# Kernel optimization log

Measured on AMD Instinct MI355X. Metric: run time of the kernel, lower is better.

## Reference

```python
import jax, jax.numpy as jnp
import numpy as np

N = 50000   # nodes
E = 800000  # edges
H = 128     # hidden_dim
K = 4       # Chebyshev order
EPS_BN = 1e-5
EPS_L2 = 1e-12


def setup_inputs() -> dict:
    key = jax.random.key(0)
    ks = jax.random.split(key, 8)
    x = jax.random.normal(ks[0], (N, 3), dtype=jnp.float32)
    edge_index = jax.random.randint(ks[1], (2, E), 0, N, dtype=jnp.int32)

    def lin(k, fi, fo):
        s = 1.0 / np.sqrt(fi)
        return jax.random.uniform(k, (fi, fo), jnp.float32, -s, s)

    def cheb_params(k, fi, fo):
        kk = jax.random.split(k, K)
        W = jnp.stack([lin(kk[i], fi, fo) for i in range(K)])  # [K, fi, fo]
        b = jnp.zeros((fo,), jnp.float32)
        return W, b

    W1, b1 = cheb_params(ks[2], 3, H)
    W2, b2 = cheb_params(ks[3], H, H)
    W3, b3 = cheb_params(ks[4], H, H)
    W4, b4 = cheb_params(ks[5], H, H)
    Wr = lin(ks[6], H, 3)
    br = jnp.zeros((3,), jnp.float32)
    ones = jnp.ones((H,), jnp.float32)
    zeros = jnp.zeros((H,), jnp.float32)
    return {
        'x': x, 'edge_index': edge_index,
        'W1': W1, 'b1': b1, 'W2': W2, 'b2': b2,
        'W3': W3, 'b3': b3, 'W4': W4, 'b4': b4,
        'g1': ones, 'be1': zeros, 'g2': ones, 'be2': zeros,
        'g3': ones, 'be3': zeros, 'Wr': Wr, 'br': br,
    }


def _prop(h, src, dst, norm):
    # one sparse Laplacian application: out[dst] += norm * h[src]
    return jax.ops.segment_sum(norm[:, None] * h[src], dst, num_segments=N)


def _cheb(h, src, dst, norm, W, b):
    # PyG ChebConv with sym normalization, lambda_max=2 -> L_hat edge weights
    # are -D^-1/2 A D^-1/2 with zero diagonal (encoded in norm).
    out = h @ W[0]
    Tx0, Tx1 = h, _prop(h, src, dst, norm)
    out = out + Tx1 @ W[1]
    for k in range(2, W.shape[0]):
        Tx2 = 2.0 * _prop(Tx1, src, dst, norm) - Tx0
        out = out + Tx2 @ W[k]
        Tx0, Tx1 = Tx1, Tx2
    return out + b


def _bn(h, g, b):
    # BatchNorm1d in training mode: batch stats over node dim, biased var
    m = h.mean(axis=0)
    v = h.var(axis=0)
    return g * (h - m) * jax.lax.rsqrt(v + EPS_BN) + b


def reference(x, edge_index, W1, b1, W2, b2, W3, b3, W4, b4,
              g1, be1, g2, be2, g3, be3, Wr, br):
    src, dst = edge_index[0], edge_index[1]
    deg = jax.ops.segment_sum(jnp.ones((E,), jnp.float32), src, num_segments=N)
    dinv = jnp.where(deg > 0, jax.lax.rsqrt(jnp.maximum(deg, 1.0)), 0.0)
    norm = -dinv[src] * dinv[dst]

    h = _bn(jax.nn.leaky_relu(_cheb(x, src, dst, norm, W1, b1)), g1, be1)
    h = _bn(jax.nn.leaky_relu(_cheb(h, src, dst, norm, W2, b2)), g2, be2)
    h = _bn(jax.nn.relu(_cheb(h, src, dst, norm, W3, b3)), g3, be3)
    h = _cheb(h, src, dst, norm, W4, b4)
    # F.normalize(p=2, dim=1)
    h = h / jnp.maximum(jnp.linalg.norm(h, axis=1, keepdims=True), EPS_L2)
    return h @ Wr + br
```

## Files before the change

### kernel.cpp

```cpp
#include <hip/hip_runtime.h>
#include <hip/hip_fp16.h>

#define HD 128

typedef __attribute__((ext_vector_type(8))) short bf16x8;
typedef __attribute__((ext_vector_type(4))) float f32x4;
typedef unsigned int u32;

struct h4s { __half2 a, b; };

__device__ __forceinline__ float lrelu(float x, float s) { return x > 0.f ? x : s * x; }

__device__ __forceinline__ u32 bf16rtne(float x) {
  u32 u = __float_as_uint(x);
  return (u + 0x7fffu + ((u >> 16) & 1u)) >> 16;
}

__global__ void k_edge_count(const int* __restrict__ src, const int* __restrict__ dst,
                             int* __restrict__ degc, int* __restrict__ cnt, int E) {
  int e = blockIdx.x * blockDim.x + threadIdx.x;
  if (e < E) {
    atomicAdd(&degc[src[e]], 1);
    atomicAdd(&cnt[dst[e]], 1);
  }
}

__global__ __launch_bounds__(1024) void k_scan1(const int* __restrict__ cnt,
                                                int* __restrict__ rowptr,
                                                int* __restrict__ bsums, int n) {
  __shared__ int buf[1024];
  int i = blockIdx.x * 1024 + threadIdx.x;
  int v = (i < n) ? cnt[i] : 0;
  buf[threadIdx.x] = v;
  __syncthreads();
  for (int o = 1; o < 1024; o <<= 1) {
    int t = (threadIdx.x >= (unsigned)o) ? buf[threadIdx.x - o] : 0;
    __syncthreads();
    buf[threadIdx.x] += t;
    __syncthreads();
  }
  if (i < n) rowptr[i] = buf[threadIdx.x] - v;
  if (threadIdx.x == 1023) bsums[blockIdx.x] = buf[1023];
}

__global__ __launch_bounds__(1024) void k_scan3(int* __restrict__ rowptr, int* __restrict__ wo,
                                                const int* __restrict__ bsums,
                                                const int* __restrict__ degc,
                                                float* __restrict__ dinv, int n, int Etot,
                                                int nb) {
  __shared__ int blockoff;
  if (nb <= 64) {
    if (threadIdx.x < 64) {
      int lane = threadIdx.x;
      int v = (lane < nb) ? bsums[lane] : 0;
      int inc = v;
#pragma unroll
      for (int o = 1; o < 64; o <<= 1) {
        int t = __shfl_up(inc, o, 64);
        if (lane >= o) inc += t;
      }
      if (lane == (int)blockIdx.x) blockoff = inc - v;
    }
  } else if (threadIdx.x == 0) {
    int sum = 0;
    for (int t = 0; t < (int)blockIdx.x; ++t) sum += bsums[t];
    blockoff = sum;
  }
  __syncthreads();
  int i = blockIdx.x * 1024 + threadIdx.x;
  if (i < n) {
    int r = rowptr[i] + blockoff;
    rowptr[i] = r;
    wo[i] = r;
    int dg = degc[i];
    dinv[i] = dg > 0 ? rsqrtf((float)dg) : 0.f;
  }
  if (i == 0) rowptr[n] = Etot;
}

__global__ void k_fill(const int* __restrict__ src, const int* __restrict__ dst,
                       int* __restrict__ wo, const float* __restrict__ dinv,
                       uint2* __restrict__ cw, int E) {
  int e = blockIdx.x * blockDim.x + threadIdx.x;
  if (e < E) {
    int s = src[e], d = dst[e];
    int p = atomicAdd(&wo[d], 1);
    cw[p] = make_uint2((u32)s, __float_as_uint(-dinv[s] * dinv[d]));
  }
}

__global__ void k_prop3(const int* __restrict__ rowptr, const uint2* __restrict__ cw,
                        const float* __restrict__ Hs, const float* __restrict__ Sub,
                        float* __restrict__ Out, float scale, int n) {
  int r = blockIdx.x * blockDim.x + threadIdx.x;
  if (r >= n) return;
  int b = rowptr[r], e = rowptr[r + 1];
  float a0 = 0.f, a1 = 0.f, a2 = 0.f;
  for (int j = b; j < e; ++j) {
    uint2 m = cw[j];
    int s = (int)m.x;
    float w = __uint_as_float(m.y);
    a0 = fmaf(w, Hs[s * 3 + 0], a0);
    a1 = fmaf(w, Hs[s * 3 + 1], a1);
    a2 = fmaf(w, Hs[s * 3 + 2], a2);
  }
  float r0 = scale * a0, r1 = scale * a1, r2 = scale * a2;
  if (Sub) { r0 -= Sub[r * 3 + 0]; r1 -= Sub[r * 3 + 1]; r2 -= Sub[r * 3 + 2]; }
  Out[r * 3 + 0] = r0; Out[r * 3 + 1] = r1; Out[r * 3 + 2] = r2;
}

template <int PHI>
__global__ __launch_bounds__(256) void k_prop128(
    const int* __restrict__ rowptr, const uint2* __restrict__ cw,
    const __half* __restrict__ Ph, const float* __restrict__ Sub,
    float* __restrict__ Out, __half* __restrict__ Outh, float scale, int n,
    const float* __restrict__ gsc, const float* __restrict__ gsh,
    const float* __restrict__ ssc, const float* __restrict__ ssh, float slope) {
  int r = blockIdx.x * 4 + (int)(threadIdx.x >> 6);
  int lane = threadIdx.x & 63;
  if (r >= n) return;
  int b = rowptr[r], e = rowptr[r + 1];
  int fl = (lane & 31) << 2;
  int half = lane >> 5;
  float ax = 0.f, ay = 0.f, az = 0.f, aw = 0.f, ws = 0.f;
  int j = b;
  for (; j + 7 < e; j += 8) {
    h4s h[4];
    float w[4];
#pragma unroll
    for (int q = 0; q < 4; ++q) {
      int idx = j + 2 * q + half;
      uint2 m = cw[idx];
      w[q] = __uint_as_float(m.y);
      h[q] = *(const h4s*)&Ph[(size_t)m.x * HD + fl];
    }
#pragma unroll
    for (int q = 0; q < 4; ++q) {
      float2 f0 = __half22float2(h[q].a);
      float2 f1 = __half22float2(h[q].b);
      if (PHI) {
        f0.x = lrelu(f0.x, slope); f0.y = lrelu(f0.y, slope);
        f1.x = lrelu(f1.x, slope); f1.y = lrelu(f1.y, slope);
        ws += w[q];
      }
      ax = fmaf(w[q], f0.x, ax);
      ay = fmaf(w[q], f0.y, ay);
      az = fmaf(w[q], f1.x, az);
      aw = fmaf(w[q], f1.y, aw);
    }
  }
  for (; j + 1 < e; j += 2) {
    int idx = j + half;
    uint2 m = cw[idx];
    float w = __uint_as_float(m.y);
    h4s h = *(const h4s*)&Ph[(size_t)m.x * HD + fl];
    float2 f0 = __half22float2(h.a);
    float2 f1 = __half22float2(h.b);
    if (PHI) {
      f0.x = lrelu(f0.x, slope); f0.y = lrelu(f0.y, slope);
      f1.x = lrelu(f1.x, slope); f1.y = lrelu(f1.y, slope);
      ws += w;
    }
    ax = fmaf(w, f0.x, ax);
    ay = fmaf(w, f0.y, ay);
    az = fmaf(w, f1.x, az);
    aw = fmaf(w, f1.y, aw);
  }
  if (j < e && half == 0) {
    uint2 m = cw[j];
    float w = __uint_as_float(m.y);
    h4s h = *(const h4s*)&Ph[(size_t)m.x * HD + fl];
    float2 f0 = __half22float2(h.a);
    float2 f1 = __half22float2(h.b);
    if (PHI) {
      f0.x = lrelu(f0.x, slope); f0.y = lrelu(f0.y, slope);
      f1.x = lrelu(f1.x, slope); f1.y = lrelu(f1.y, slope);
      ws += w;
    }
    ax = fmaf(w, f0.x, ax);
    ay = fmaf(w, f0.y, ay);
    az = fmaf(w, f1.x, az);
    aw = fmaf(w, f1.y, aw);
  }
  ax += __shfl_xor(ax, 32, 64);
  ay += __shfl_xor(ay, 32, 64);
  az += __shfl_xor(az, 32, 64);
  aw += __shfl_xor(aw, 32, 64);
  if (PHI) {
    ws += __shfl_xor(ws, 32, 64);
    float4 g4 = *(const float4*)&gsc[fl];
    float4 s4 = *(const float4*)&gsh[fl];
    ax = fmaf(ax, g4.x, ws * s4.x);
    ay = fmaf(ay, g4.y, ws * s4.y);
    az = fmaf(az, g4.z, ws * s4.z);
    aw = fmaf(aw, g4.w, ws * s4.w);
  }
  float4 o = make_float4(scale * ax, scale * ay, scale * az, scale * aw);
  if (Sub) {
    float4 sb = *(const float4*)&Sub[(size_t)r * HD + fl];
    if (ssc != nullptr) {
      float4 c4 = *(const float4*)&ssc[fl];
      float4 d4 = *(const float4*)&ssh[fl];
      sb.x = fmaf(lrelu(sb.x, slope), c4.x, d4.x);
      sb.y = fmaf(lrelu(sb.y, slope), c4.y, d4.y);
      sb.z = fmaf(lrelu(sb.z, slope), c4.z, d4.z);
      sb.w = fmaf(lrelu(sb.w, slope), c4.w, d4.w);
    }
    o.x -= sb.x; o.y -= sb.y; o.z -= sb.z; o.w -= sb.w;
  }
  if (half == 0) {
    *(float4*)&Out[(size_t)r * HD + fl] = o;
    if (Outh) {
      h4s ho;
      ho.a = __float22half2_rn(make_float2(o.x, o.y));
      ho.b = __float22half2_rn(make_float2(o.z, o.w));
      *(h4s*)&Outh[(size_t)r * HD + fl] = ho;
    }
  }
}

__global__ __launch_bounds__(128) void k_l1gemm(
    const float* __restrict__ X, const float* __restrict__ T1, const float* __restrict__ T2,
    const float* __restrict__ T3, const float* __restrict__ W1, const float* __restrict__ b1,
    float* __restrict__ Out, __half* __restrict__ Outh,
    float* __restrict__ bnsum, float* __restrict__ bnsq,
    float slope, int n, int rpb) {
  int j = threadIdx.x;
  float w[12];
#pragma unroll
  for (int t = 0; t < 4; ++t)
#pragma unroll
    for (int c = 0; c < 3; ++c) w[t * 3 + c] = W1[(t * 3 + c) * HD + j];
  float bj = b1[j];
  int r0 = blockIdx.x * rpb, r1 = min(r0 + rpb, n);
  float s = 0.f, q = 0.f;
  for (int r = r0; r < r1; ++r) {
    float acc = bj;
#pragma unroll
    for (int c = 0; c < 3; ++c) {
      acc = fmaf(X [r * 3 + c], w[0 + c], acc);
      acc = fmaf(T1[r * 3 + c], w[3 + c], acc);
      acc = fmaf(T2[r * 3 + c], w[6 + c], acc);
      acc = fmaf(T3[r * 3 + c], w[9 + c], acc);
    }
    Out[(size_t)r * HD + j] = acc;
    Outh[(size_t)r * HD + j] = __float2half(acc);
    float a = lrelu(acc, slope);
    s += a;
    q = fmaf(a, a, q);
  }
  atomicAdd(&bnsum[j], s);
  atomicAdd(&bnsq[j], q);
}

__global__ void k_wsplit3(const float* __restrict__ W2, const float* __restrict__ W3,
                          const float* __restrict__ W4, uint4* __restrict__ Whi,
                          uint4* __restrict__ Wlo) {
  int flat = blockIdx.x * 256 + threadIdx.x;
  int wsel = flat >> 13;
  int f = flat & 8191;
  const float* W = (wsel == 0) ? W2 : (wsel == 1) ? W3 : W4;
  int n = f & 127, K8 = f >> 7;
  int chunk = K8 >> 2, g = K8 & 3;
  bf16x8 hv, lv;
#pragma unroll
  for (int i = 0; i < 8; ++i) {
    int k = chunk * 32 + ((i >> 2) << 4) + g * 4 + (i & 3);
    float v = W[(size_t)k * HD + n];
    u32 hb = bf16rtne(v);
    float hf = __uint_as_float(hb << 16);
    u32 lb = bf16rtne(v - hf);
    hv[i] = (short)hb;
    lv[i] = (short)lb;
  }
  int slot = chunk * 512 + (n >> 4) * 64 + g * 16 + (n & 15);
  Whi[wsel * 8192 + slot] = *(uint4*)&hv;
  Wlo[wsel * 8192 + slot] = *(uint4*)&lv;
}

__global__ __launch_bounds__(256) void k_gemm4m(
    const float* __restrict__ T0, const float* __restrict__ T1,
    const float* __restrict__ T2, const float* __restrict__ T3,
    const uint4* __restrict__ Whi, const uint4* __restrict__ Wlo,
    const float* __restrict__ bias, float* __restrict__ OUT, __half* __restrict__ OUTh,
    float* bnsum, float* bnsq, float stat_slope,
    const float* __restrict__ gsc, const float* __restrict__ gsh, float phi_slope,
    int nrows) {
  __shared__ short sAh[2048], sAl[2048];
  __shared__ short sWh[4096], sWl[4096];
  __shared__ float redS[128], redQ[128];

  int tid = threadIdx.x;
  int lane = tid & 63, w = tid >> 6, wr = w >> 1, wc = w & 1;
  int g = (tid >> 4) & 3;
  int ri = tid & 15;
  int row0 = blockIdx.x * 64;
  int arow = row0 + w * 16 + ri;
  bool aval = arow < nrows;

  f32x4 zero = {0.f, 0.f, 0.f, 0.f};
  f32x4 acc[2][4];
#pragma unroll
  for (int mi = 0; mi < 2; ++mi)
#pragma unroll
    for (int nj = 0; nj < 4; ++nj) acc[mi][nj] = zero;

  if (tid < 128) { redS[tid] = 0.f; redQ[tid] = 0.f; }

  for (int chunk = 0; chunk < 16; ++chunk) {
    const float* Ts = (chunk < 4) ? T0 : (chunk < 8) ? T1 : (chunk < 12) ? T2 : T3;
    int kc = chunk & 3;
    float4 va = make_float4(0.f, 0.f, 0.f, 0.f), vb = va;
    if (aval) {
      const float* ap = Ts + (size_t)arow * HD + kc * 32 + g * 4;
      va = *(const float4*)ap;
      vb = *(const float4*)(ap + 16);
    }
    size_t wbase = (size_t)chunk * 512;
    uint4 wh0 = Whi[wbase + tid], wh1 = Whi[wbase + 256 + tid];
    uint4 wl0 = Wlo[wbase + tid], wl1 = Wlo[wbase + 256 + tid];

    __syncthreads();

    float vals[8] = {va.x, va.y, va.z, va.w, vb.x, vb.y, vb.z, vb.w};
    if (gsc != nullptr && chunk < 4) {
#pragma unroll
      for (int i = 0; i < 8; ++i) {
        int f = kc * 32 + g * 4 + (i & 3) + ((i >> 2) << 4);
        vals[i] = fmaf(lrelu(vals[i], phi_slope), gsc[f], gsh[f]);
      }
    }
    bf16x8 hv, lv;
#pragma unroll
    for (int i = 0; i < 8; ++i) {
      u32 hb = bf16rtne(vals[i]);
      float hf = __uint_as_float(hb << 16);
      u32 lb = bf16rtne(vals[i] - hf);
      hv[i] = (short)hb;
      lv[i] = (short)lb;
    }
    *(bf16x8*)&sAh[tid * 8] = hv;
    *(bf16x8*)&sAl[tid * 8] = lv;
    *(uint4*)&sWh[tid * 8] = wh0;
    *(uint4*)&sWh[(256 + tid) * 8] = wh1;
    *(uint4*)&sWl[tid * 8] = wl0;
    *(uint4*)&sWl[(256 + tid) * 8] = wl1;
    __syncthreads();

    bf16x8 ah[2], al[2], bh[4], bl[4];
#pragma unroll
    for (int mi = 0; mi < 2; ++mi) {
      ah[mi] = *(const bf16x8*)&sAh[((wr * 2 + mi) * 64 + lane) * 8];
      al[mi] = *(const bf16x8*)&sAl[((wr * 2 + mi) * 64 + lane) * 8];
    }
#pragma unroll
    for (int nj = 0; nj < 4; ++nj) {
      bh[nj] = *(const bf16x8*)&sWh[((wc * 4 + nj) * 64 + lane) * 8];
      bl[nj] = *(const bf16x8*)&sWl[((wc * 4 + nj) * 64 + lane) * 8];
    }
#pragma unroll
    for (int mi = 0; mi < 2; ++mi)
#pragma unroll
      for (int nj = 0; nj < 4; ++nj) {
        acc[mi][nj] = __builtin_amdgcn_mfma_f32_16x16x32_bf16(ah[mi], bh[nj], acc[mi][nj], 0, 0, 0);
        acc[mi][nj] = __builtin_amdgcn_mfma_f32_16x16x32_bf16(ah[mi], bl[nj], acc[mi][nj], 0, 0, 0);
        acc[mi][nj] = __builtin_amdgcn_mfma_f32_16x16x32_bf16(al[mi], bh[nj], acc[mi][nj], 0, 0, 0);
      }
  }

  int l4 = (lane >> 4) * 4, ni = lane & 15;
  bool stats = (bnsum != nullptr);
#pragma unroll
  for (int nj = 0; nj < 4; ++nj) {
    int c = wc * 64 + nj * 16 + ni;
    float bcol = bias[c];
    float s = 0.f, q = 0.f;
#pragma unroll
    for (int mi = 0; mi < 2; ++mi)
#pragma unroll
      for (int j = 0; j < 4; ++j) {
        int row = row0 + (wr * 2 + mi) * 16 + l4 + j;
        if (row < nrows) {
          float v = acc[mi][nj][j] + bcol;
          OUT[(size_t)row * HD + c] = v;
          if (OUTh) OUTh[(size_t)row * HD + c] = __float2half(v);
          if (stats) {
            float a = lrelu(v, stat_slope);
            s += a;
            q = fmaf(a, a, q);
          }
        }
      }
    if (stats) {
      s += __shfl_xor(s, 16, 64);
      s += __shfl_xor(s, 32, 64);
      q += __shfl_xor(q, 16, 64);
      q += __shfl_xor(q, 32, 64);
      if (lane < 16) {
        atomicAdd(&redS[c], s);
        atomicAdd(&redQ[c], q);
      }
    }
  }
  if (stats) {
    __syncthreads();
    if (tid < 128) {
      atomicAdd(&bnsum[tid], redS[tid]);
      atomicAdd(&bnsq[tid], redQ[tid]);
    }
  }
}

__global__ void k_bnfin(const float* __restrict__ bsum, const float* __restrict__ bsq,
                        const float* __restrict__ g, const float* __restrict__ be,
                        float* __restrict__ scaleb, float* __restrict__ shiftb, int n) {
  int f = threadIdx.x;
  if (f < HD) {
    float m = bsum[f] / (float)n;
    float v = bsq[f] / (float)n - m * m;
    float rs = rsqrtf(v + 1e-5f);
    float sc = g[f] * rs;
    scaleb[f] = sc;
    shiftb[f] = be[f] - m * sc;
  }
}

__global__ __launch_bounds__(256) void k_final(const float* __restrict__ Hb,
                                               const float* __restrict__ Wr,
                                               const float* __restrict__ br,
                                               float* __restrict__ out, int n) {
  int r = blockIdx.x * 4 + (int)(threadIdx.x >> 6);
  int lane = threadIdx.x & 63;
  if (r >= n) return;
  float h0 = Hb[(size_t)r * HD + lane];
  float h1 = Hb[(size_t)r * HD + 64 + lane];
  float ss = h0 * h0 + h1 * h1;
#pragma unroll
  for (int o = 32; o; o >>= 1) ss += __shfl_xor(ss, o, 64);
  float inv = 1.f / fmaxf(sqrtf(ss), 1e-12f);
  h0 *= inv; h1 *= inv;
  float o0 = h0 * Wr[lane * 3 + 0] + h1 * Wr[(64 + lane) * 3 + 0];
  float o1 = h0 * Wr[lane * 3 + 1] + h1 * Wr[(64 + lane) * 3 + 1];
  float o2 = h0 * Wr[lane * 3 + 2] + h1 * Wr[(64 + lane) * 3 + 2];
#pragma unroll
  for (int o = 32; o; o >>= 1) {
    o0 += __shfl_xor(o0, o, 64);
    o1 += __shfl_xor(o1, o, 64);
    o2 += __shfl_xor(o2, o, 64);
  }
  if (lane == 0) {
    out[r * 3 + 0] = o0 + br[0];
    out[r * 3 + 1] = o1 + br[1];
    out[r * 3 + 2] = o2 + br[2];
  }
}

extern "C" void kernel_launch(void* const* d_in, const int* in_sizes, int n_in,
                              void* d_out, int out_size, void* d_ws, size_t ws_size,
                              hipStream_t stream) {
  const float* x  = (const float*)d_in[0];
  const int*   ei = (const int*)d_in[1];
  const float* W1 = (const float*)d_in[2];
  const float* b1 = (const float*)d_in[3];
  const float* W2 = (const float*)d_in[4];
  const float* b2 = (const float*)d_in[5];
  const float* W3 = (const float*)d_in[6];
  const float* b3 = (const float*)d_in[7];
  const float* W4 = (const float*)d_in[8];
  const float* b4 = (const float*)d_in[9];
  const float* g1 = (const float*)d_in[10];
  const float* be1= (const float*)d_in[11];
  const float* g2 = (const float*)d_in[12];
  const float* be2= (const float*)d_in[13];
  const float* g3 = (const float*)d_in[14];
  const float* be3= (const float*)d_in[15];
  const float* Wr = (const float*)d_in[16];
  const float* br = (const float*)d_in[17];

  const int N = in_sizes[0] / 3;
  const int E = in_sizes[1] / 2;
  const int* src = ei;
  const int* dst = ei + E;
  float* out = (float*)d_out;

  char* wp = (char*)d_ws;
  size_t used = 0;
  auto alloc = [&](size_t bytes) -> void* {
    void* p = (void*)(wp + used);
    used += (bytes + 255) & ~(size_t)255;
    return p;
  };
  int*   deg2   = (int*)alloc((size_t)2 * N * 4);
  int*   rowptr = (int*)alloc((size_t)(N + 1) * 4);
  int*   wo     = (int*)alloc((size_t)N * 4);
  float* dinv   = (float*)alloc((size_t)N * 4);
  int*   bsums  = (int*)alloc(256 * 4);
  uint2* cw     = (uint2*)alloc((size_t)E * 8);
  float* t1     = (float*)alloc((size_t)N * 3 * 4);
  float* t2     = (float*)alloc((size_t)N * 3 * 4);
  float* t3     = (float*)alloc((size_t)N * 3 * 4);
  float* buf0   = (float*)alloc((size_t)N * HD * 4);
  float* buf1   = (float*)alloc((size_t)N * HD * 4);
  float* buf2   = (float*)alloc((size_t)N * HD * 4);
  float* buf3   = (float*)alloc((size_t)N * HD * 4);
  __half* phA   = (__half*)alloc((size_t)N * HD * 2);
  __half* phB   = (__half*)alloc((size_t)N * HD * 2);
  float* stats  = (float*)alloc(6 * HD * 4);
  float* scsh   = (float*)alloc(6 * HD * 4);
  uint4* Whi3   = (uint4*)alloc(3 * 8192 * 16);
  uint4* Wlo3   = (uint4*)alloc(3 * 8192 * 16);
  if (used > ws_size) return;

  int* degc = deg2;
  int* cnt  = deg2 + N;
  float* bnsum1 = stats + 0 * HD; float* bnsq1 = stats + 1 * HD;
  float* bnsum2 = stats + 2 * HD; float* bnsq2 = stats + 3 * HD;
  float* bnsum3 = stats + 4 * HD; float* bnsq3 = stats + 5 * HD;
  float* sc1 = scsh + 0 * HD; float* sh1 = scsh + 1 * HD;
  float* sc2 = scsh + 2 * HD; float* sh2 = scsh + 3 * HD;
  float* sc3 = scsh + 4 * HD; float* sh3 = scsh + 5 * HD;

  const int eb = (E + 255) / 256;
  const int nb = (N + 255) / 256;
  const int pb = (N + 3) / 4;
  const int sb = (N + 1023) / 1024;
  const int gbm = (N + 63) / 64;

  hipMemsetAsync(stats, 0, 6 * HD * 4, stream);
  hipMemsetAsync(deg2, 0, (size_t)2 * N * 4, stream);
  k_edge_count<<<eb, 256, 0, stream>>>(src, dst, degc, cnt, E);
  k_scan1<<<sb, 1024, 0, stream>>>(cnt, rowptr, bsums, N);
  k_scan3<<<sb, 1024, 0, stream>>>(rowptr, wo, bsums, degc, dinv, N, E, sb);
  k_fill<<<eb, 256, 0, stream>>>(src, dst, wo, dinv, cw, E);
  k_wsplit3<<<96, 256, 0, stream>>>(W2, W3, W4, Whi3, Wlo3);

  k_prop3<<<nb, 256, 0, stream>>>(rowptr, cw, x, nullptr, t1, 1.f, N);
  k_prop3<<<nb, 256, 0, stream>>>(rowptr, cw, t1, x, t2, 2.f, N);
  k_prop3<<<nb, 256, 0, stream>>>(rowptr, cw, t2, t1, t3, 2.f, N);
  k_l1gemm<<<(N + 255) / 256, 128, 0, stream>>>(x, t1, t2, t3, W1, b1, buf0, phA,
                                                bnsum1, bnsq1, 0.01f, N, 256);
  k_bnfin<<<1, 128, 0, stream>>>(bnsum1, bnsq1, g1, be1, sc1, sh1, N);

  auto cheb_layer = [&](const uint4* Whi, const uint4* Wlo, const float* bk,
                        const float* psc, const float* psh, float phi_slope,
                        float* bs, float* bq, float stat_slope, bool last) {
    k_prop128<1><<<pb, 256, 0, stream>>>(rowptr, cw, phA, nullptr, buf1, phB, 1.f, N,
                                         psc, psh, nullptr, nullptr, phi_slope);
    k_prop128<0><<<pb, 256, 0, stream>>>(rowptr, cw, phB, buf0, buf2, phA, 2.f, N,
                                         nullptr, nullptr, psc, psh, phi_slope);
    k_prop128<0><<<pb, 256, 0, stream>>>(rowptr, cw, phA, buf1, buf3, nullptr, 2.f, N,
                                         nullptr, nullptr, nullptr, nullptr, 0.f);
    k_gemm4m<<<gbm, 256, 0, stream>>>(buf0, buf1, buf2, buf3, Whi, Wlo, bk, buf0,
                                      last ? nullptr : phA,
                                      bs, bq, stat_slope, psc, psh, phi_slope, N);
  };

  cheb_layer(Whi3, Wlo3, b2, sc1, sh1, 0.01f, bnsum2, bnsq2, 0.01f, false);
  k_bnfin<<<1, 128, 0, stream>>>(bnsum2, bnsq2, g2, be2, sc2, sh2, N);
  cheb_layer(Whi3 + 8192, Wlo3 + 8192, b3, sc2, sh2, 0.01f, bnsum3, bnsq3, 0.0f, false);
  k_bnfin<<<1, 128, 0, stream>>>(bnsum3, bnsq3, g3, be3, sc3, sh3, N);
  cheb_layer(Whi3 + 16384, Wlo3 + 16384, b4, sc3, sh3, 0.0f, nullptr, nullptr, 0.0f, true);

  k_final<<<pb, 256, 0, stream>>>(buf0, Wr, br, out, N);
}
```

Before: 721.2 us.

## Store all Chebyshev intermediates in fp16 and drop atomic CSR fill

Removes the fp32 copies of the Chebyshev intermediates. The propagation, GEMM and final kernels now read and write only fp16 buffers (four half buffers rotated per layer), roughly halving intermediate memory traffic. The CSR build also records each edge's slot from the counting atomic, so the fill pass computes positions without a second atomic. This trades some precision, since the subtracted terms and the GEMM inputs are now fp16-rounded, and adds an E-sized index buffer.

Result: faster. 684.8 us (-5.0%).

```diff
diff --git a/kernel.cpp b/kernel.cpp
--- a/kernel.cpp
+++ b/kernel.cpp
@@ -17,11 +17,12 @@
 }
 
 __global__ void k_edge_count(const int* __restrict__ src, const int* __restrict__ dst,
-                             int* __restrict__ degc, int* __restrict__ cnt, int E) {
+                             int* __restrict__ degc, int* __restrict__ cnt,
+                             int* __restrict__ ledge, int E) {
   int e = blockIdx.x * blockDim.x + threadIdx.x;
   if (e < E) {
     atomicAdd(&degc[src[e]], 1);
-    atomicAdd(&cnt[dst[e]], 1);
+    ledge[e] = atomicAdd(&cnt[dst[e]], 1);
   }
 }
 
@@ -43,7 +44,7 @@
   if (threadIdx.x == 1023) bsums[blockIdx.x] = buf[1023];
 }
 
-__global__ __launch_bounds__(1024) void k_scan3(int* __restrict__ rowptr, int* __restrict__ wo,
+__global__ __launch_bounds__(1024) void k_scan3(int* __restrict__ rowptr,
                                                 const int* __restrict__ bsums,
                                                 const int* __restrict__ degc,
                                                 float* __restrict__ dinv, int n, int Etot,
@@ -69,9 +70,7 @@
   __syncthreads();
   int i = blockIdx.x * 1024 + threadIdx.x;
   if (i < n) {
-    int r = rowptr[i] + blockoff;
-    rowptr[i] = r;
-    wo[i] = r;
+    rowptr[i] += blockoff;
     int dg = degc[i];
     dinv[i] = dg > 0 ? rsqrtf((float)dg) : 0.f;
   }
@@ -79,12 +78,12 @@
 }
 
 __global__ void k_fill(const int* __restrict__ src, const int* __restrict__ dst,
-                       int* __restrict__ wo, const float* __restrict__ dinv,
-                       uint2* __restrict__ cw, int E) {
+                       const int* __restrict__ ledge, const int* __restrict__ rowptr,
+                       const float* __restrict__ dinv, uint2* __restrict__ cw, int E) {
   int e = blockIdx.x * blockDim.x + threadIdx.x;
   if (e < E) {
     int s = src[e], d = dst[e];
-    int p = atomicAdd(&wo[d], 1);
+    int p = rowptr[d] + ledge[e];
     cw[p] = make_uint2((u32)s, __float_as_uint(-dinv[s] * dinv[d]));
   }
 }
@@ -112,8 +111,8 @@
 template <int PHI>
 __global__ __launch_bounds__(256) void k_prop128(
     const int* __restrict__ rowptr, const uint2* __restrict__ cw,
-    const __half* __restrict__ Ph, const float* __restrict__ Sub,
-    float* __restrict__ Out, __half* __restrict__ Outh, float scale, int n,
+    const __half* __restrict__ Ph, const __half* __restrict__ Sub,
+    __half* __restrict__ Outh, float scale, int n,
     const float* __restrict__ gsc, const float* __restrict__ gsh,
     const float* __restrict__ ssc, const float* __restrict__ ssh, float slope) {
   int r = blockIdx.x * 4 + (int)(threadIdx.x >> 6);
@@ -197,33 +196,31 @@
   }
   float4 o = make_float4(scale * ax, scale * ay, scale * az, scale * aw);
   if (Sub) {
-    float4 sb = *(const float4*)&Sub[(size_t)r * HD + fl];
+    h4s sh4 = *(const h4s*)&Sub[(size_t)r * HD + fl];
+    float2 s0 = __half22float2(sh4.a);
+    float2 s1 = __half22float2(sh4.b);
     if (ssc != nullptr) {
       float4 c4 = *(const float4*)&ssc[fl];
       float4 d4 = *(const float4*)&ssh[fl];
-      sb.x = fmaf(lrelu(sb.x, slope), c4.x, d4.x);
-      sb.y = fmaf(lrelu(sb.y, slope), c4.y, d4.y);
-      sb.z = fmaf(lrelu(sb.z, slope), c4.z, d4.z);
-      sb.w = fmaf(lrelu(sb.w, slope), c4.w, d4.w);
-    }
-    o.x -= sb.x; o.y -= sb.y; o.z -= sb.z; o.w -= sb.w;
+      s0.x = fmaf(lrelu(s0.x, slope), c4.x, d4.x);
+      s0.y = fmaf(lrelu(s0.y, slope), c4.y, d4.y);
+      s1.x = fmaf(lrelu(s1.x, slope), c4.z, d4.z);
+      s1.y = fmaf(lrelu(s1.y, slope), c4.w, d4.w);
+    }
+    o.x -= s0.x; o.y -= s0.y; o.z -= s1.x; o.w -= s1.y;
   }
   if (half == 0) {
-    *(float4*)&Out[(size_t)r * HD + fl] = o;
-    if (Outh) {
-      h4s ho;
-      ho.a = __float22half2_rn(make_float2(o.x, o.y));
-      ho.b = __float22half2_rn(make_float2(o.z, o.w));
-      *(h4s*)&Outh[(size_t)r * HD + fl] = ho;
-    }
+    h4s ho;
+    ho.a = __float22half2_rn(make_float2(o.x, o.y));
+    ho.b = __float22half2_rn(make_float2(o.z, o.w));
+    *(h4s*)&Outh[(size_t)r * HD + fl] = ho;
   }
 }
 
 __global__ __launch_bounds__(128) void k_l1gemm(
     const float* __restrict__ X, const float* __restrict__ T1, const float* __restrict__ T2,
     const float* __restrict__ T3, const float* __restrict__ W1, const float* __restrict__ b1,
-    float* __restrict__ Out, __half* __restrict__ Outh,
-    float* __restrict__ bnsum, float* __restrict__ bnsq,
+    __half* __restrict__ Outh, float* __restrict__ bnsum, float* __restrict__ bnsq,
     float slope, int n, int rpb) {
   int j = threadIdx.x;
   float w[12];
@@ -243,7 +240,6 @@
       acc = fmaf(T2[r * 3 + c], w[6 + c], acc);
       acc = fmaf(T3[r * 3 + c], w[9 + c], acc);
     }
-    Out[(size_t)r * HD + j] = acc;
     Outh[(size_t)r * HD + j] = __float2half(acc);
     float a = lrelu(acc, slope);
     s += a;
@@ -279,10 +275,10 @@
 }
 
 __global__ __launch_bounds__(256) void k_gemm4m(
-    const float* __restrict__ T0, const float* __restrict__ T1,
-    const float* __restrict__ T2, const float* __restrict__ T3,
+    const __half* __restrict__ T0, const __half* __restrict__ T1,
+    const __half* __restrict__ T2, const __half* __restrict__ T3,
     const uint4* __restrict__ Whi, const uint4* __restrict__ Wlo,
-    const float* __restrict__ bias, float* __restrict__ OUT, __half* __restrict__ OUTh,
+    const float* __restrict__ bias, __half* __restrict__ OUTh,
     float* bnsum, float* bnsq, float stat_slope,
     const float* __restrict__ gsc, const float* __restrict__ gsh, float phi_slope,
     int nrows) {
@@ -308,13 +304,17 @@
   if (tid < 128) { redS[tid] = 0.f; redQ[tid] = 0.f; }
 
   for (int chunk = 0; chunk < 16; ++chunk) {
-    const float* Ts = (chunk < 4) ? T0 : (chunk < 8) ? T1 : (chunk < 12) ? T2 : T3;
+    const __half* Ts = (chunk < 4) ? T0 : (chunk < 8) ? T1 : (chunk < 12) ? T2 : T3;
     int kc = chunk & 3;
-    float4 va = make_float4(0.f, 0.f, 0.f, 0.f), vb = va;
+    float vals[8] = {0.f, 0.f, 0.f, 0.f, 0.f, 0.f, 0.f, 0.f};
     if (aval) {
-      const float* ap = Ts + (size_t)arow * HD + kc * 32 + g * 4;
-      va = *(const float4*)ap;
-      vb = *(const float4*)(ap + 16);
+      const __half* ap = Ts + (size_t)arow * HD + kc * 32 + g * 4;
+      h4s va = *(const h4s*)ap;
+      h4s vb = *(const h4s*)(ap + 16);
+      float2 f0 = __half22float2(va.a), f1 = __half22float2(va.b);
+      float2 f2 = __half22float2(vb.a), f3 = __half22float2(vb.b);
+      vals[0] = f0.x; vals[1] = f0.y; vals[2] = f1.x; vals[3] = f1.y;
+      vals[4] = f2.x; vals[5] = f2.y; vals[6] = f3.x; vals[7] = f3.y;
     }
     size_t wbase = (size_t)chunk * 512;
     uint4 wh0 = Whi[wbase + tid], wh1 = Whi[wbase + 256 + tid];
@@ -322,7 +322,6 @@
 
     __syncthreads();
 
-    float vals[8] = {va.x, va.y, va.z, va.w, vb.x, vb.y, vb.z, vb.w};
     if (gsc != nullptr && chunk < 4) {
 #pragma unroll
       for (int i = 0; i < 8; ++i) {
@@ -382,8 +381,7 @@
         int row = row0 + (wr * 2 + mi) * 16 + l4 + j;
         if (row < nrows) {
           float v = acc[mi][nj][j] + bcol;
-          OUT[(size_t)row * HD + c] = v;
-          if (OUTh) OUTh[(size_t)row * HD + c] = __float2half(v);
+          OUTh[(size_t)row * HD + c] = __float2half(v);
           if (stats) {
             float a = lrelu(v, stat_slope);
             s += a;
@@ -425,15 +423,15 @@
   }
 }
 
-__global__ __launch_bounds__(256) void k_final(const float* __restrict__ Hb,
+__global__ __launch_bounds__(256) void k_final(const __half* __restrict__ Hb,
                                                const float* __restrict__ Wr,
                                                const float* __restrict__ br,
                                                float* __restrict__ out, int n) {
   int r = blockIdx.x * 4 + (int)(threadIdx.x >> 6);
   int lane = threadIdx.x & 63;
   if (r >= n) return;
-  float h0 = Hb[(size_t)r * HD + lane];
-  float h1 = Hb[(size_t)r * HD + 64 + lane];
+  float h0 = __half2float(Hb[(size_t)r * HD + lane]);
+  float h1 = __half2float(Hb[(size_t)r * HD + 64 + lane]);
   float ss = h0 * h0 + h1 * h1;
 #pragma unroll
   for (int o = 32; o; o >>= 1) ss += __shfl_xor(ss, o, 64);
@@ -492,19 +490,17 @@
   };
   int*   deg2   = (int*)alloc((size_t)2 * N * 4);
   int*   rowptr = (int*)alloc((size_t)(N + 1) * 4);
-  int*   wo     = (int*)alloc((size_t)N * 4);
   float* dinv   = (float*)alloc((size_t)N * 4);
   int*   bsums  = (int*)alloc(256 * 4);
+  int*   ledge  = (int*)alloc((size_t)E * 4);
   uint2* cw     = (uint2*)alloc((size_t)E * 8);
   float* t1     = (float*)alloc((size_t)N * 3 * 4);
   float* t2     = (float*)alloc((size_t)N * 3 * 4);
   float* t3     = (float*)alloc((size_t)N * 3 * 4);
-  float* buf0   = (float*)alloc((size_t)N * HD * 4);
-  float* buf1   = (float*)alloc((size_t)N * HD * 4);
-  float* buf2   = (float*)alloc((size_t)N * HD * 4);
-  float* buf3   = (float*)alloc((size_t)N * HD * 4);
   __half* phA   = (__half*)alloc((size_t)N * HD * 2);
   __half* phB   = (__half*)alloc((size_t)N * HD * 2);
+  __half* phC   = (__half*)alloc((size_t)N * HD * 2);
+  __half* phD   = (__half*)alloc((size_t)N * HD * 2);
   float* stats  = (float*)alloc(6 * HD * 4);
   float* scsh   = (float*)alloc(6 * HD * 4);
   uint4* Whi3   = (uint4*)alloc(3 * 8192 * 16);
@@ -528,38 +524,37 @@
 
   hipMemsetAsync(stats, 0, 6 * HD * 4, stream);
   hipMemsetAsync(deg2, 0, (size_t)2 * N * 4, stream);
-  k_edge_count<<<eb, 256, 0, stream>>>(src, dst, degc, cnt, E);
+  k_edge_count<<<eb, 256, 0, stream>>>(src, dst, degc, cnt, ledge, E);
   k_scan1<<<sb, 1024, 0, stream>>>(cnt, rowptr, bsums, N);
-  k_scan3<<<sb, 1024, 0, stream>>>(rowptr, wo, bsums, degc, dinv, N, E, sb);
-  k_fill<<<eb, 256, 0, stream>>>(src, dst, wo, dinv, cw, E);
+  k_scan3<<<sb, 1024, 0, stream>>>(rowptr, bsums, degc, dinv, N, E, sb);
+  k_fill<<<eb, 256, 0, stream>>>(src, dst, ledge, rowptr, dinv, cw, E);
   k_wsplit3<<<96, 256, 0, stream>>>(W2, W3, W4, Whi3, Wlo3);
 
   k_prop3<<<nb, 256, 0, stream>>>(rowptr, cw, x, nullptr, t1, 1.f, N);
   k_prop3<<<nb, 256, 0, stream>>>(rowptr, cw, t1, x, t2, 2.f, N);
   k_prop3<<<nb, 256, 0, stream>>>(rowptr, cw, t2, t1, t3, 2.f, N);
-  k_l1gemm<<<(N + 255) / 256, 128, 0, stream>>>(x, t1, t2, t3, W1, b1, buf0, phA,
+  k_l1gemm<<<(N + 255) / 256, 128, 0, stream>>>(x, t1, t2, t3, W1, b1, phA,
                                                 bnsum1, bnsq1, 0.01f, N, 256);
   k_bnfin<<<1, 128, 0, stream>>>(bnsum1, bnsq1, g1, be1, sc1, sh1, N);
 
   auto cheb_layer = [&](const uint4* Whi, const uint4* Wlo, const float* bk,
                         const float* psc, const float* psh, float phi_slope,
-                        float* bs, float* bq, float stat_slope, bool last) {
-    k_prop128<1><<<pb, 256, 0, stream>>>(rowptr, cw, phA, nullptr, buf1, phB, 1.f, N,
+                        float* bs, float* bq, float stat_slope) {
+    k_prop128<1><<<pb, 256, 0, stream>>>(rowptr, cw, phA, nullptr, phB, 1.f, N,
                                          psc, psh, nullptr, nullptr, phi_slope);
-    k_prop128<0><<<pb, 256, 0, stream>>>(rowptr, cw, phB, buf0, buf2, phA, 2.f, N,
+    k_prop128<0><<<pb, 256, 0, stream>>>(rowptr, cw, phB, phA, phC, 2.f, N,
                                          nullptr, nullptr, psc, psh, phi_slope);
-    k_prop128<0><<<pb, 256, 0, stream>>>(rowptr, cw, phA, buf1, buf3, nullptr, 2.f, N,
+    k_prop128<0><<<pb, 256, 0, stream>>>(rowptr, cw, phC, phB, phD, 2.f, N,
                                          nullptr, nullptr, nullptr, nullptr, 0.f);
-    k_gemm4m<<<gbm, 256, 0, stream>>>(buf0, buf1, buf2, buf3, Whi, Wlo, bk, buf0,
-                                      last ? nullptr : phA,
+    k_gemm4m<<<gbm, 256, 0, stream>>>(phA, phB, phC, phD, Whi, Wlo, bk, phA,
                                       bs, bq, stat_slope, psc, psh, phi_slope, N);
   };
 
-  cheb_layer(Whi3, Wlo3, b2, sc1, sh1, 0.01f, bnsum2, bnsq2, 0.01f, false);
+  cheb_layer(Whi3, Wlo3, b2, sc1, sh1, 0.01f, bnsum2, bnsq2, 0.01f);
   k_bnfin<<<1, 128, 0, stream>>>(bnsum2, bnsq2, g2, be2, sc2, sh2, N);
-  cheb_layer(Whi3 + 8192, Wlo3 + 8192, b3, sc2, sh2, 0.01f, bnsum3, bnsq3, 0.0f, false);
+  cheb_layer(Whi3 + 8192, Wlo3 + 8192, b3, sc2, sh2, 0.01f, bnsum3, bnsq3, 0.0f);
   k_bnfin<<<1, 128, 0, stream>>>(bnsum3, bnsq3, g3, be3, sc3, sh3, N);
-  cheb_layer(Whi3 + 16384, Wlo3 + 16384, b4, sc3, sh3, 0.0f, nullptr, nullptr, 0.0f, true);
-
-  k_final<<<pb, 256, 0, stream>>>(buf0, Wr, br, out, N);
-}
+  cheb_layer(Whi3 + 16384, Wlo3 + 16384, b4, sc3, sh3, 0.0f, nullptr, nullptr, 0.0f);
+
+  k_final<<<pb, 256, 0, stream>>>(phA, Wr, br, out, N);
+}
```
